# Kernel optimization log

Measured on AMD Instinct MI355X. Metric: run time of the kernel, lower is better.

The kernel has to match this reference:

```python
import jax, jax.numpy as jnp
import numpy as np

N, D = 8192, 512
NUM_SOURCES = 8


def setup_inputs() -> dict:
    key = jax.random.key(0)
    k1, k2, k3 = jax.random.split(key, 3)
    image_features = jax.random.normal(k1, (N, D), dtype=jnp.float32)
    text_features = jax.random.normal(k2, (N, D), dtype=jnp.float32)
    logit_scale = jnp.ones((), dtype=jnp.float32)
    source_labels = jax.random.randint(k3, (N,), 0, NUM_SOURCES, dtype=jnp.int64)
    return {
        "image_features": image_features,
        "text_features": text_features,
        "logit_scale": logit_scale,
        "source_labels": source_labels,
    }


def reference(image_features, text_features, logit_scale, source_labels):
    n = source_labels.shape[0]
    # [N, N] logits and row-wise log-softmax
    logits = logit_scale * (image_features @ text_features.T)
    log_probs = jax.nn.log_softmax(logits, axis=1)
    # same-source mask, diagonal excluded
    mask = (source_labels[:, None] == source_labels[None, :]) & (~jnp.eye(n, dtype=bool))
    count_pos = mask.sum(axis=1)  # [N]
    row_sum = jnp.where(mask, log_probs, 0.0).sum(axis=1)  # [N]
    # per-row mean over positives; rows with zero positives contribute 0
    row_mean = jnp.where(count_pos > 0, row_sum / jnp.maximum(count_pos, 1).astype(log_probs.dtype), 0.0)
    # loss = -(sum_i row_mean_i) / N
    return -row_mean.sum() / n
```

## Files before the change

kernel.cpp:

```cpp
#include <hip/hip_runtime.h>
#include <cmath>

#define NN 8192
#define DD 512
#define NSRC 8
#define PSW 8
#define COFF 100.0f

typedef __bf16 bf16x8 __attribute__((ext_vector_type(8)));
typedef float  f32x4  __attribute__((ext_vector_type(4)));

__device__ __forceinline__ unsigned short f2bf(float f) {
    unsigned u = __float_as_uint(f);
    u += 0x7fffu + ((u >> 16) & 1u);
    return (unsigned short)(u >> 16);
}

__global__ __launch_bounds__(256) void k_prep(
    const float* __restrict__ img, const float* __restrict__ txt,
    const int* __restrict__ labels,
    unsigned short* __restrict__ imgB, unsigned short* __restrict__ txtB,
    float* __restrict__ Tsum, int* __restrict__ counts,
    float* __restrict__ dsv)
{
    const int tid = threadIdx.x;
    if (blockIdx.x >= 128) {
        const int wv   = tid >> 6;
        const int lane = tid & 63;
        const int row  = (blockIdx.x - 128) * 4 + wv;
        const size_t base = (size_t)row * DD + lane * 8;
        const float4 i0 = *(const float4*)(img + base);
        const float4 i1 = *(const float4*)(img + base + 4);
        const float4 t0 = *(const float4*)(txt + base);
        const float4 t1 = *(const float4*)(txt + base + 4);
        union { unsigned short s[8]; uint4 v; } oi, ot;
        oi.s[0] = f2bf(i0.x); oi.s[1] = f2bf(i0.y); oi.s[2] = f2bf(i0.z); oi.s[3] = f2bf(i0.w);
        oi.s[4] = f2bf(i1.x); oi.s[5] = f2bf(i1.y); oi.s[6] = f2bf(i1.z); oi.s[7] = f2bf(i1.w);
        ot.s[0] = f2bf(t0.x); ot.s[1] = f2bf(t0.y); ot.s[2] = f2bf(t0.z); ot.s[3] = f2bf(t0.w);
        ot.s[4] = f2bf(t1.x); ot.s[5] = f2bf(t1.y); ot.s[6] = f2bf(t1.z); ot.s[7] = f2bf(t1.w);
        *(uint4*)(imgB + base) = oi.v;
        *(uint4*)(txtB + base) = ot.v;
        float ds = i0.x * t0.x + i0.y * t0.y + i0.z * t0.z + i0.w * t0.w
                 + i1.x * t1.x + i1.y * t1.y + i1.z * t1.z + i1.w * t1.w;
#pragma unroll
        for (int off = 32; off; off >>= 1) ds += __shfl_xor(ds, off);
        if (lane == 0) dsv[row] = ds;
        return;
    }
    __shared__ float Tacc[NSRC * DD];
    __shared__ int cacc[NSRC];
    const int d0 = 2 * tid;
#pragma unroll
    for (int s = 0; s < NSRC; s++) {
        Tacc[s * DD + d0] = 0.f;
        Tacc[s * DD + d0 + 1] = 0.f;
    }
    if (tid < NSRC) cacc[tid] = 0;
    __syncthreads();

    const int row0 = blockIdx.x * 64;
    if (tid < 64) atomicAdd(&cacc[labels[row0 + tid]], 1);

    for (int j = 0; j < 64; j++) {
        const int lab = labels[row0 + j];
        const float2 v = *(const float2*)(txt + (size_t)(row0 + j) * DD + d0);
        Tacc[lab * DD + d0]     += v.x;
        Tacc[lab * DD + d0 + 1] += v.y;
    }
    __syncthreads();
#pragma unroll
    for (int k = 0; k < NSRC * DD / 256; k++) {
        const int e = k * 256 + tid;
        atomicAdd(&Tsum[e], Tacc[e]);
    }
    if (tid < NSRC) atomicAdd(&counts[tid], cacc[tid]);
}

__global__ __launch_bounds__(512, 2) void k_lse_mfma256(
    const unsigned short* __restrict__ imgB, const unsigned short* __restrict__ txtB,
    const float* __restrict__ scale_p, float* __restrict__ ps)
{
    __shared__ uint4 lds[8192];
    const float scale = scale_p[0];
    const int tid  = threadIdx.x;
    const int lane = tid & 63;
    const int w    = tid >> 6;
    const int wr   = w >> 1;
    const int wc   = w & 1;
    const int lq   = lane >> 4;
    const int ln   = lane & 15;
    const int c    = blockIdx.x & 7;
    const int l    = blockIdx.x >> 3;
    const int by   = c * 4 + (l >> 3);
    const int bcg  = l & 7;
    const int row0    = by * 256;
    const int colBase = bcg * 1024;

    const int st_r  = tid >> 3;
    const int st_kc = (tid & 7) ^ (st_r & 7);
    const int xsw   = ln & 7;

    int aA[2][2], aB[2][2];
#pragma unroll
    for (int b = 0; b < 2; b++)
#pragma unroll
        for (int ks = 0; ks < 2; ks++) {
            const int perm = ((ks << 2) + lq) ^ xsw;
            aA[b][ks] = b * 65536 + (wr * 64 + ln) * 128 + perm * 16;
            aB[b][ks] = b * 65536 + 32768 + (wc * 128 + ln) * 128 + perm * 16;
        }
    const unsigned short* gA0 = imgB + (size_t)(row0 + st_r) * DD + (st_kc << 3);
    const unsigned short* gB0 = txtB + (size_t)(colBase + st_r) * DD + (st_kc << 3);

#define SA(BUF, Q, T)                                                          \
    { const unsigned short* g = gA0 + ((Q) << 15) + (((T) & 7) << 6);          \
      __builtin_amdgcn_global_load_lds(                                        \
          (const __attribute__((address_space(1))) void*)g,                    \
          (__attribute__((address_space(3))) void*)                            \
              &lds[(BUF) * 4096 + (Q) * 512 + tid], 16, 0, 0); }
#define SB(BUF, Q, T)                                                          \
    { const unsigned short* g = gB0 + ((size_t)(((T) >> 3) & 3) << 17)         \
          + ((Q) << 15) + (((T) & 7) << 6);                                    \
      __builtin_amdgcn_global_load_lds(                                        \
          (const __attribute__((address_space(1))) void*)g,                    \
          (__attribute__((address_space(3))) void*)                            \
              &lds[(BUF) * 4096 + 2048 + (Q) * 512 + tid], 16, 0, 0); }

#define PH_(BUF, JH, RA, STG)                                                  \
    do {                                                                       \
        if (RA) {                                                              \
            _Pragma("unroll") for (int ks = 0; ks < 2; ks++)                   \
                _Pragma("unroll") for (int ii = 0; ii < 4; ii++)               \
                    af[ii][ks] = *reinterpret_cast<const bf16x8*>(             \
                        (const char*)lds + aA[BUF][ks] + ii * 2048);           \
        }                                                                      \
        bf16x8 bf[2][2];                                                       \
        _Pragma("unroll") for (int ks = 0; ks < 2; ks++)                       \
            _Pragma("unroll") for (int jj = 0; jj < 2; jj++)                   \
                bf[jj][ks] = *reinterpret_cast<const bf16x8*>(                 \
                    (const char*)lds + aB[BUF][ks] + (JH) * 4096 + jj * 2048); \
        STG;                                                                   \
        __builtin_amdgcn_sched_barrier(0);                                     \
        __builtin_amdgcn_s_setprio(1);                                         \
        _Pragma("unroll") for (int ks = 0; ks < 2; ks++) {                     \
            _Pragma("unroll") for (int ii = 0; ii < 4; ii++) {                 \
                _Pragma("unroll") for (int jj = 0; jj < 2; jj++) {             \
                    acc[ii][(JH) * 2 + jj] =                                   \
                        __builtin_amdgcn_mfma_f32_16x16x32_bf16(               \
                            af[ii][ks], bf[jj][ks], acc[ii][(JH) * 2 + jj],    \
                            0, 0, 0);                                          \
                }                                                              \
            }                                                                  \
        }                                                                      \
        __builtin_amdgcn_s_setprio(0);                                         \
    } while (0)

#pragma unroll
    for (int q = 0; q < 4; q++) SA(0, q, 0);
#pragma unroll
    for (int q = 0; q < 4; q++) SB(0, q, 0);
    SA(1, 0, 1); SA(1, 2, 1);
    asm volatile("s_waitcnt vmcnt(2)" ::: "memory");
    __builtin_amdgcn_s_barrier();

    f32x4 acc[4][8];
    f32x4 s_run[4];
#pragma unroll
    for (int i = 0; i < 4; i++) {
        s_run[i] = (f32x4){0.f, 0.f, 0.f, 0.f};
#pragma unroll
        for (int j = 0; j < 8; j++) acc[i][j] = (f32x4){0.f, 0.f, 0.f, 0.f};
    }
    bf16x8 af[4][2];

#pragma unroll 1
    for (int v0 = 0; v0 < 32; v0 += 2) {
        PH_(0, 0, 1,
            SA(1, 1, v0 + 1); SA(1, 3, v0 + 1);
            SB(1, 0, v0 + 1); SB(1, 1, v0 + 1);
            SB(1, 2, v0 + 1); SB(1, 3, v0 + 1));
        PH_(0, 1, 0, (void)0);
        __builtin_amdgcn_s_barrier();
        PH_(0, 2, 0, SA(0, 0, v0 + 2); SA(0, 2, v0 + 2));
        PH_(0, 3, 0, (void)0);
        asm volatile("s_waitcnt vmcnt(2)" ::: "memory");
        __builtin_amdgcn_s_barrier();
        PH_(1, 0, 1,
            SA(0, 1, v0 + 2); SA(0, 3, v0 + 2);
            SB(0, 0, v0 + 2); SB(0, 1, v0 + 2);
            SB(0, 2, v0 + 2); SB(0, 3, v0 + 2));
        PH_(1, 1, 0, (void)0);
        __builtin_amdgcn_s_barrier();
        PH_(1, 2, 0, SA(1, 0, v0 + 3); SA(1, 2, v0 + 3));
        PH_(1, 3, 0, (void)0);
        asm volatile("s_waitcnt vmcnt(2)" ::: "memory");
        __builtin_amdgcn_s_barrier();
        if ((v0 & 6) == 6) {
#pragma unroll
            for (int i = 0; i < 4; i++) {
#pragma unroll
                for (int rg = 0; rg < 4; rg++) {
                    float es = s_run[i][rg];
#pragma unroll
                    for (int j = 0; j < 8; j++)
                        es += __expf(fmaf(acc[i][j][rg], scale, -COFF));
                    s_run[i][rg] = es;
                }
#pragma unroll
                for (int j = 0; j < 8; j++)
                    acc[i][j] = (f32x4){0.f, 0.f, 0.f, 0.f};
            }
        }
    }

    asm volatile("s_waitcnt vmcnt(0)" ::: "memory");
    __syncthreads();

    float* fred = (float*)lds;
#pragma unroll
    for (int i = 0; i < 4; i++) {
#pragma unroll
        for (int rg = 0; rg < 4; rg++) {
            float es = s_run[i][rg];
#pragma unroll
            for (int off = 8; off; off >>= 1) es += __shfl_xor(es, off);
            if (ln == 0)
                fred[(wr * 64 + i * 16 + lq * 4 + rg) * 2 + wc] = es;
        }
    }
    __syncthreads();
    if (tid < 256) {
        const float tot = fred[tid * 2] + fred[tid * 2 + 1];
        ps[(size_t)(row0 + tid) * PSW + bcg] = tot;
    }
#undef SA
#undef SB
#undef PH_
}

__global__ __launch_bounds__(256) void k_finalize(
    const unsigned short* __restrict__ imgB,
    const int* __restrict__ labels, const float* __restrict__ scale_p,
    const float* __restrict__ Tsum, const int* __restrict__ counts,
    const float* __restrict__ ps, const float* __restrict__ dsv,
    float* __restrict__ out)
{
    const float scale = scale_p[0];
    const int tid = threadIdx.x;
    const int lane = tid & 63;
    const int wave = tid >> 6;
    const int rowBase = blockIdx.x * 16 + wave * 4;
    float local = 0.f;
#pragma unroll
    for (int it = 0; it < 4; it++) {
        const int i = rowBase + it;
        const int lab = labels[i];
        const float* sp = Tsum + lab * DD + lane * 8;
        union { uint4 v; unsigned short s[8]; } iv;
        iv.v = *(const uint4*)(imgB + (size_t)i * DD + lane * 8);
        const float4 s0 = *(const float4*)(sp);
        const float4 s1 = *(const float4*)(sp + 4);
        float dt = 0.f;
        dt = fmaf(__uint_as_float((unsigned)iv.s[0] << 16), s0.x, dt);
        dt = fmaf(__uint_as_float((unsigned)iv.s[1] << 16), s0.y, dt);
        dt = fmaf(__uint_as_float((unsigned)iv.s[2] << 16), s0.z, dt);
        dt = fmaf(__uint_as_float((unsigned)iv.s[3] << 16), s0.w, dt);
        dt = fmaf(__uint_as_float((unsigned)iv.s[4] << 16), s1.x, dt);
        dt = fmaf(__uint_as_float((unsigned)iv.s[5] << 16), s1.y, dt);
        dt = fmaf(__uint_as_float((unsigned)iv.s[6] << 16), s1.z, dt);
        dt = fmaf(__uint_as_float((unsigned)iv.s[7] << 16), s1.w, dt);
        float es = (lane < PSW) ? ps[(size_t)i * PSW + lane] : 0.f;
#pragma unroll
        for (int off = 32; off; off >>= 1) {
            dt += __shfl_xor(dt, off);
            es += __shfl_xor(es, off);
        }
        if (lane == 0) {
            const float lse = COFF + __logf(es);
            const int cnt = counts[lab] - 1;
            if (cnt > 0) {
                const float row_sum = scale * (dt - dsv[i]) - (float)cnt * lse;
                local += row_sum / (float)cnt;
            }
        }
    }
    __shared__ float red[4];
    if (lane == 0) red[wave] = local;
    __syncthreads();
    if (tid == 0) {
        const float t = red[0] + red[1] + red[2] + red[3];
        atomicAdd(out, -t / (float)NN);
    }
}

extern "C" void kernel_launch(void* const* d_in, const int* in_sizes, int n_in,
                              void* d_out, int out_size, void* d_ws, size_t ws_size,
                              hipStream_t stream)
{
    const float* img     = (const float*)d_in[0];
    const float* txt     = (const float*)d_in[1];
    const float* scale_p = (const float*)d_in[2];
    const int*   labels  = (const int*)d_in[3];
    float* out = (float*)d_out;

    char* ws = (char*)d_ws;
    float* ps    = (float*)(ws);
    float* Tsum  = (float*)(ws + (1 << 18));
    int*   counts = (int*)(ws + (1 << 18) + NSRC * DD * 4);
    float* dsv   = (float*)(ws + 0x48000);
    unsigned short* imgB = (unsigned short*)(ws + 2 * 1024 * 1024);
    unsigned short* txtB = (unsigned short*)(ws + 10 * 1024 * 1024);

    hipMemsetAsync(ws + (1 << 18), 0, NSRC * DD * 4 + 64, stream);
    hipMemsetAsync(d_out, 0, 4, stream);

    k_prep<<<128 + NN / 4, 256, 0, stream>>>(
        img, txt, labels, imgB, txtB, Tsum, counts, dsv);
    k_lse_mfma256<<<256, 512, 0, stream>>>(imgB, txtB, scale_p, ps);
    k_finalize<<<NN / 16, 256, 0, stream>>>(imgB, labels, scale_p,
                                            Tsum, counts, ps, dsv, out);
}
```

Before: 157.4 us.

## Simplify GEMM staging to whole-tile double buffering and fold output zeroing into prep

```diff
diff --git a/kernel.cpp b/kernel.cpp
--- a/kernel.cpp
+++ b/kernel.cpp
@@ -21,10 +21,11 @@
     const int* __restrict__ labels,
     unsigned short* __restrict__ imgB, unsigned short* __restrict__ txtB,
     float* __restrict__ Tsum, int* __restrict__ counts,
-    float* __restrict__ dsv)
+    float* __restrict__ dsv, float* __restrict__ out)
 {
     const int tid = threadIdx.x;
     if (blockIdx.x >= 128) {
+        if (blockIdx.x == 128 && tid == 0) out[0] = 0.f;
         const int wv   = tid >> 6;
         const int lane = tid & 63;
         const int row  = (blockIdx.x - 128) * 4 + wv;
@@ -125,6 +126,10 @@
           (const __attribute__((address_space(1))) void*)g,                    \
           (__attribute__((address_space(3))) void*)                            \
               &lds[(BUF) * 4096 + 2048 + (Q) * 512 + tid], 16, 0, 0); }
+
+#define STG8(BUF, T)                                                           \
+    SA(BUF, 0, T); SA(BUF, 1, T); SA(BUF, 2, T); SA(BUF, 3, T);                \
+    SB(BUF, 0, T); SB(BUF, 1, T); SB(BUF, 2, T); SB(BUF, 3, T)
 
 #define PH_(BUF, JH, RA, STG)                                                  \
     do {                                                                       \
@@ -155,12 +160,8 @@
         __builtin_amdgcn_s_setprio(0);                                         \
     } while (0)
 
-#pragma unroll
-    for (int q = 0; q < 4; q++) SA(0, q, 0);
-#pragma unroll
-    for (int q = 0; q < 4; q++) SB(0, q, 0);
-    SA(1, 0, 1); SA(1, 2, 1);
-    asm volatile("s_waitcnt vmcnt(2)" ::: "memory");
+    STG8(0, 0);
+    asm volatile("s_waitcnt vmcnt(0)" ::: "memory");
     __builtin_amdgcn_s_barrier();
 
     f32x4 acc[4][8];
@@ -175,25 +176,17 @@
 
 #pragma unroll 1
     for (int v0 = 0; v0 < 32; v0 += 2) {
-        PH_(0, 0, 1,
-            SA(1, 1, v0 + 1); SA(1, 3, v0 + 1);
-            SB(1, 0, v0 + 1); SB(1, 1, v0 + 1);
-            SB(1, 2, v0 + 1); SB(1, 3, v0 + 1));
+        PH_(0, 0, 1, STG8(1, v0 + 1));
         PH_(0, 1, 0, (void)0);
+        PH_(0, 2, 0, (void)0);
+        PH_(0, 3, 0, (void)0);
+        asm volatile("s_waitcnt vmcnt(0)" ::: "memory");
         __builtin_amdgcn_s_barrier();
-        PH_(0, 2, 0, SA(0, 0, v0 + 2); SA(0, 2, v0 + 2));
-        PH_(0, 3, 0, (void)0);
-        asm volatile("s_waitcnt vmcnt(2)" ::: "memory");
-        __builtin_amdgcn_s_barrier();
-        PH_(1, 0, 1,
-            SA(0, 1, v0 + 2); SA(0, 3, v0 + 2);
-            SB(0, 0, v0 + 2); SB(0, 1, v0 + 2);
-            SB(0, 2, v0 + 2); SB(0, 3, v0 + 2));
+        PH_(1, 0, 1, STG8(0, v0 + 2));
         PH_(1, 1, 0, (void)0);
-        __builtin_amdgcn_s_barrier();
-        PH_(1, 2, 0, SA(1, 0, v0 + 3); SA(1, 2, v0 + 3));
+        PH_(1, 2, 0, (void)0);
         PH_(1, 3, 0, (void)0);
-        asm volatile("s_waitcnt vmcnt(2)" ::: "memory");
+        asm volatile("s_waitcnt vmcnt(0)" ::: "memory");
         __builtin_amdgcn_s_barrier();
         if ((v0 & 6) == 6) {
 #pragma unroll
@@ -213,7 +206,6 @@
         }
     }
 
-    asm volatile("s_waitcnt vmcnt(0)" ::: "memory");
     __syncthreads();
 
     float* fred = (float*)lds;
@@ -235,6 +227,7 @@
     }
 #undef SA
 #undef SB
+#undef STG8
 #undef PH_
 }
 
@@ -312,10 +305,9 @@
     unsigned short* txtB = (unsigned short*)(ws + 10 * 1024 * 1024);
 
     hipMemsetAsync(ws + (1 << 18), 0, NSRC * DD * 4 + 64, stream);
-    hipMemsetAsync(d_out, 0, 4, stream);
 
     k_prep<<<128 + NN / 4, 256, 0, stream>>>(
-        img, txt, labels, imgB, txtB, Tsum, counts, dsv);
+        img, txt, labels, imgB, txtB, Tsum, counts, dsv, out);
     k_lse_mfma256<<<256, 512, 0, stream>>>(imgB, txtB, scale_p, ps);
     k_finalize<<<NN / 16, 256, 0, stream>>>(imgB, labels, scale_p,
                                             Tsum, counts, ps, dsv, out);
```

Result: no change. 155.8 us, median of 2 (-1.0%).
